# Performance work log

Measured on AMD Instinct MI355X. Metric: run time of the kernel, lower is better.

## Reference

```python
import jax, jax.numpy as jnp
import numpy as np

N_LEVELS = 7  # log2(64) + 1

def setup_inputs() -> dict:
    key = jax.random.key(0)
    k1, k2, k3 = jax.random.split(key, 3)
    B, C, H, W = 32, 3, 64, 64
    flat_dim = C  # patch_size = 1
    n_embd = 896
    inner = n_embd // N_LEVELS  # 128
    return {
        "x": jax.random.normal(k1, (B, C, H, W), dtype=jnp.float32),
        "emb_w": jax.random.normal(k2, (flat_dim * N_LEVELS, n_embd), dtype=jnp.float32) * 0.05,
        "emb_b": jnp.zeros((n_embd,), dtype=jnp.float32),
        "cls_w": jax.random.normal(k3, (inner, 1000), dtype=jnp.float32) * 0.05,
        "cls_b": jnp.zeros((1000,), dtype=jnp.float32),
    }

def _token_tree(xp):
    # xp: (B, H, W, fd). For level l, every token gets the mean of its
    # aligned 2^l x 2^l block (quad-tree pooling), broadcast back to HxW.
    B, H, W, fd = xp.shape
    levels = []
    for l in range(N_LEVELS):
        bs = 2 ** l
        m = xp.reshape(B, H // bs, bs, W // bs, bs, fd).mean(axis=(2, 4))
        m = jnp.repeat(jnp.repeat(m, bs, axis=1), bs, axis=2)
        levels.append(m)
    return jnp.stack(levels, axis=3)  # (B, H, W, L, fd)

def reference(x, emb_w, emb_b, cls_w, cls_b):
    B, C, H, W = x.shape
    # patch extraction with patch_size=1 -> (B, H, W, C)
    xp = jnp.transpose(x, (0, 2, 3, 1))
    tree = _token_tree(xp)                      # (B,H,W,L,fd)
    flat = tree.reshape(B, H, W, -1)            # (B,H,W,L*fd)
    emb = flat @ emb_w + emb_b                  # (B,H,W,n_embd)
    inner = emb.shape[-1] // N_LEVELS
    emb = emb.reshape(B, H, W, N_LEVELS, inner)
    # num_layers = 0 -> nn.Sequential() is identity
    root = emb[:, :, :, N_LEVELS - 1, :]        # (B,H,W,inner)
    root_avg = root.mean(axis=(1, 2))           # (B,inner)
    return root_avg @ cls_w + cls_b             # (B,1000)
```

## Files before the change

### kernel.cpp

```cpp
#include <hip/hip_runtime.h>

#define BATCH   32
#define CHANS   3
#define HW      4096
#define NLEV    7
#define NEMBD   896
#define INNER   128
#define ROOTOFF 768
#define NCLS    1000

__global__ void k_reduce_x(const float* __restrict__ x, float* __restrict__ g) {
    const int bc = blockIdx.x;
    const float4* p4 = (const float4*)(x + (size_t)bc * HW);
    const int t = threadIdx.x;
    float s = 0.f;
#pragma unroll
    for (int i = 0; i < 4; ++i) {
        float4 v = p4[t + 256 * i];
        s += (v.x + v.y) + (v.z + v.w);
    }
#pragma unroll
    for (int off = 32; off > 0; off >>= 1)
        s += __shfl_down(s, off, 64);
    __shared__ float ls[4];
    if ((t & 63) == 0) ls[t >> 6] = s;
    __syncthreads();
    if (t == 0)
        g[bc] = (ls[0] + ls[1] + ls[2] + ls[3]) * (1.0f / HW);
}

__global__ void k_head(const float* __restrict__ g,
                       const float* __restrict__ emb_w,
                       const float* __restrict__ emb_b,
                       const float* __restrict__ cls_w,
                       const float* __restrict__ cls_b,
                       float* __restrict__ out) {
    const int b = blockIdx.y;
    const int t = threadIdx.x;
    __shared__ float ra[INNER];

    if (t < INNER) {
        float acc = emb_b[ROOTOFF + t];
#pragma unroll
        for (int c = 0; c < CHANS; ++c) {
            float w = 0.f;
#pragma unroll
            for (int l = 0; l < NLEV; ++l)
                w += emb_w[(size_t)(l * CHANS + c) * NEMBD + ROOTOFF + t];
            acc += g[b * CHANS + c] * w;
        }
        ra[t] = acc;
    }
    __syncthreads();

    const int k = blockIdx.x * blockDim.x + t;
    if (k < NCLS) {
        float acc = cls_b[k];
#pragma unroll 8
        for (int j = 0; j < INNER; ++j)
            acc += ra[j] * cls_w[(size_t)j * NCLS + k];
        out[(size_t)b * NCLS + k] = acc;
    }
}

extern "C" void kernel_launch(void* const* d_in, const int* in_sizes, int n_in,
                              void* d_out, int out_size, void* d_ws, size_t ws_size,
                              hipStream_t stream) {
    const float* x     = (const float*)d_in[0];
    const float* emb_w = (const float*)d_in[1];
    const float* emb_b = (const float*)d_in[2];
    const float* cls_w = (const float*)d_in[3];
    const float* cls_b = (const float*)d_in[4];
    float* out = (float*)d_out;
    float* g   = (float*)d_ws;

    k_reduce_x<<<BATCH * CHANS, 256, 0, stream>>>(x, g);
    k_head<<<dim3(4, BATCH), 256, 0, stream>>>(g, emb_w, emb_b, cls_w, cls_b, out);
}
```

Measured before the change: 69.61 us.

## Fuse channel reduction and head into one kernel per batch

Replaces the two kernels (per-channel mean reduction, then embedding plus classifier head) with one kernel of 32 blocks of 1024 threads, one block per batch item. Each block reduces all three channels in shared memory and then computes the root embedding and all 1000 logits in place. This removes a kernel launch and the workspace round-trip. In exchange, parallelism drops from 96+128 blocks to 32 blocks, and each thread now runs the full 128-step classifier dot product.

```diff
diff --git a/kernel.cpp b/kernel.cpp
--- a/kernel.cpp
+++ b/kernel.cpp
@@ -9,35 +9,45 @@
 #define ROOTOFF 768
 #define NCLS    1000
 
-__global__ void k_reduce_x(const float* __restrict__ x, float* __restrict__ g) {
-    const int bc = blockIdx.x;
-    const float4* p4 = (const float4*)(x + (size_t)bc * HW);
+__global__ __launch_bounds__(1024) void k_fused(
+        const float* __restrict__ x,
+        const float* __restrict__ emb_w,
+        const float* __restrict__ emb_b,
+        const float* __restrict__ cls_w,
+        const float* __restrict__ cls_b,
+        float* __restrict__ out) {
+    const int b = blockIdx.x;
     const int t = threadIdx.x;
-    float s = 0.f;
+
+    __shared__ float wsum[16][3];
+    __shared__ float gsh[3];
+    __shared__ float ra[INNER];
+
+    const float4* p4 = (const float4*)(x + (size_t)b * (CHANS * HW));
+    float4 v0 = p4[t];
+    float4 v1 = p4[t + 1024];
+    float4 v2 = p4[t + 2048];
+    float s0 = (v0.x + v0.y) + (v0.z + v0.w);
+    float s1 = (v1.x + v1.y) + (v1.z + v1.w);
+    float s2 = (v2.x + v2.y) + (v2.z + v2.w);
 #pragma unroll
-    for (int i = 0; i < 4; ++i) {
-        float4 v = p4[t + 256 * i];
-        s += (v.x + v.y) + (v.z + v.w);
+    for (int off = 32; off > 0; off >>= 1) {
+        s0 += __shfl_down(s0, off, 64);
+        s1 += __shfl_down(s1, off, 64);
+        s2 += __shfl_down(s2, off, 64);
     }
+    const int wave = t >> 6;
+    if ((t & 63) == 0) {
+        wsum[wave][0] = s0; wsum[wave][1] = s1; wsum[wave][2] = s2;
+    }
+    __syncthreads();
+    if (t < CHANS) {
+        float acc = 0.f;
 #pragma unroll
-    for (int off = 32; off > 0; off >>= 1)
-        s += __shfl_down(s, off, 64);
-    __shared__ float ls[4];
-    if ((t & 63) == 0) ls[t >> 6] = s;
+        for (int w = 0; w < 16; ++w) acc += wsum[w][t];
+        gsh[t] = acc * (1.0f / HW);
+    }
     __syncthreads();
-    if (t == 0)
-        g[bc] = (ls[0] + ls[1] + ls[2] + ls[3]) * (1.0f / HW);
-}
-
-__global__ void k_head(const float* __restrict__ g,
-                       const float* __restrict__ emb_w,
-                       const float* __restrict__ emb_b,
-                       const float* __restrict__ cls_w,
-                       const float* __restrict__ cls_b,
-                       float* __restrict__ out) {
-    const int b = blockIdx.y;
-    const int t = threadIdx.x;
-    __shared__ float ra[INNER];
 
     if (t < INNER) {
         float acc = emb_b[ROOTOFF + t];
@@ -47,19 +57,18 @@
 #pragma unroll
             for (int l = 0; l < NLEV; ++l)
                 w += emb_w[(size_t)(l * CHANS + c) * NEMBD + ROOTOFF + t];
-            acc += g[b * CHANS + c] * w;
+            acc += gsh[c] * w;
         }
         ra[t] = acc;
     }
     __syncthreads();
 
-    const int k = blockIdx.x * blockDim.x + t;
-    if (k < NCLS) {
-        float acc = cls_b[k];
+    if (t < NCLS) {
+        float acc = cls_b[t];
 #pragma unroll 8
         for (int j = 0; j < INNER; ++j)
-            acc += ra[j] * cls_w[(size_t)j * NCLS + k];
-        out[(size_t)b * NCLS + k] = acc;
+            acc += ra[j] * cls_w[(size_t)j * NCLS + t];
+        out[(size_t)b * NCLS + t] = acc;
     }
 }
 
@@ -72,8 +81,6 @@
     const float* cls_w = (const float*)d_in[3];
     const float* cls_b = (const float*)d_in[4];
     float* out = (float*)d_out;
-    float* g   = (float*)d_ws;
 
-    k_reduce_x<<<BATCH * CHANS, 256, 0, stream>>>(x, g);
-    k_head<<<dim3(4, BATCH), 256, 0, stream>>>(g, emb_w, emb_b, cls_w, cls_b, out);
+    k_fused<<<BATCH, 1024, 0, stream>>>(x, emb_w, emb_b, cls_w, cls_b, out);
 }
```

New measurement: 68.54 us. Within noise of the previous version (-1.5%).

## Fold emb weights into classifier per class, share across batch in head kernel

Applied to the files above, without the earlier changes.

Restructures the head kernel by precomputing, per class k, three channel projections and a bias term (W_c·cls_w and emb_b·cls_w). The batch-specific output then becomes a 3-term dot product with the pooled means. Work moves from a per-batch 128-length matvec to a per-class reduction split across 16 thread rows, with a grid of 63 blocks instead of 128. This removes the redundant per-batch reads of cls_w but adds shared-memory reductions and extra syncs.

```diff
diff --git a/kernel.cpp b/kernel.cpp
--- a/kernel.cpp
+++ b/kernel.cpp
@@ -8,6 +8,7 @@
 #define INNER   128
 #define ROOTOFF 768
 #define NCLS    1000
+
 
 __global__ void k_reduce_x(const float* __restrict__ x, float* __restrict__ g) {
     const int bc = blockIdx.x;
@@ -29,37 +30,78 @@
         g[bc] = (ls[0] + ls[1] + ls[2] + ls[3]) * (1.0f / HW);
 }
 
-__global__ void k_head(const float* __restrict__ g,
-                       const float* __restrict__ emb_w,
-                       const float* __restrict__ emb_b,
-                       const float* __restrict__ cls_w,
-                       const float* __restrict__ cls_b,
-                       float* __restrict__ out) {
-    const int b = blockIdx.y;
-    const int t = threadIdx.x;
-    __shared__ float ra[INNER];
+__global__ __launch_bounds__(256) void k_head(
+        const float* __restrict__ g,
+        const float* __restrict__ emb_w,
+        const float* __restrict__ emb_b,
+        const float* __restrict__ cls_w,
+        const float* __restrict__ cls_b,
+        float* __restrict__ out) {
+    const int t  = threadIdx.x;
+    const int tx = t & 15;
+    const int ty = t >> 4;
+    const int k  = blockIdx.x * 16 + tx;
+    const bool kok = (k < NCLS);
+
+    __shared__ float wf0[INNER], wf1[INNER], wf2[INNER], eb[INNER];
+    __shared__ float gsh[BATCH * CHANS];
+    __shared__ float4 red[16][16];
+    __shared__ float4 fin[16];
 
     if (t < INNER) {
-        float acc = emb_b[ROOTOFF + t];
+        float a0 = 0.f, a1 = 0.f, a2 = 0.f;
 #pragma unroll
-        for (int c = 0; c < CHANS; ++c) {
-            float w = 0.f;
-#pragma unroll
-            for (int l = 0; l < NLEV; ++l)
-                w += emb_w[(size_t)(l * CHANS + c) * NEMBD + ROOTOFF + t];
-            acc += g[b * CHANS + c] * w;
+        for (int l = 0; l < NLEV; ++l) {
+            const float* row = emb_w + (size_t)(l * CHANS) * NEMBD + ROOTOFF + t;
+            a0 += row[0 * NEMBD];
+            a1 += row[1 * NEMBD];
+            a2 += row[2 * NEMBD];
         }
-        ra[t] = acc;
+        wf0[t] = a0; wf1[t] = a1; wf2[t] = a2;
+        eb[t]  = emb_b[ROOTOFF + t];
+    } else if (t < INNER + BATCH * CHANS) {
+        gsh[t - INNER] = g[t - INNER];
     }
     __syncthreads();
 
-    const int k = blockIdx.x * blockDim.x + t;
-    if (k < NCLS) {
-        float acc = cls_b[k];
-#pragma unroll 8
-        for (int j = 0; j < INNER; ++j)
-            acc += ra[j] * cls_w[(size_t)j * NCLS + k];
-        out[(size_t)b * NCLS + k] = acc;
+    float m0 = 0.f, m1 = 0.f, m2 = 0.f, dd = 0.f;
+    if (kok) {
+        const int jb = ty * 8;
+        float w[8];
+#pragma unroll
+        for (int jj = 0; jj < 8; ++jj)
+            w[jj] = cls_w[(size_t)(jb + jj) * NCLS + k];
+#pragma unroll
+        for (int jj = 0; jj < 8; ++jj) {
+            const int j = jb + jj;
+            m0 += wf0[j] * w[jj];
+            m1 += wf1[j] * w[jj];
+            m2 += wf2[j] * w[jj];
+            dd += eb[j]  * w[jj];
+        }
+    }
+    red[ty][tx] = make_float4(m0, m1, m2, dd);
+    __syncthreads();
+
+    if (ty == 0) {
+        float4 a = make_float4(0.f, 0.f, 0.f, kok ? cls_b[k] : 0.f);
+#pragma unroll
+        for (int yy = 0; yy < 16; ++yy) {
+            float4 p = red[yy][tx];
+            a.x += p.x; a.y += p.y; a.z += p.z; a.w += p.w;
+        }
+        fin[tx] = a;
+    }
+    __syncthreads();
+
+    if (kok) {
+        const float4 m = fin[tx];
+#pragma unroll
+        for (int h = 0; h < 2; ++h) {
+            const int b = ty + 16 * h;
+            const float* gb = gsh + b * CHANS;
+            out[(size_t)b * NCLS + k] = m.w + gb[0] * m.x + gb[1] * m.y + gb[2] * m.z;
+        }
     }
 }
 
@@ -75,5 +117,5 @@
     float* g   = (float*)d_ws;
 
     k_reduce_x<<<BATCH * CHANS, 256, 0, stream>>>(x, g);
-    k_head<<<dim3(4, BATCH), 256, 0, stream>>>(g, emb_w, emb_b, cls_w, cls_b, out);
+    k_head<<<(NCLS + 15) / 16, 256, 0, stream>>>(g, emb_w, emb_b, cls_w, cls_b, out);
 }
```

After: 64.93 us. -6.7%, faster.
